# Performance work log

Hardware: AMD Instinct MI355X
Metric: run time of the kernel (lower is better)

The kernel has to match this reference:

```python
import jax, jax.numpy as jnp
import numpy as np

N_NODES = 100000


def setup_inputs() -> dict:
    key = jax.random.key(0)
    k1, k2, k3, k4, k5 = jax.random.split(key, 5)
    x = jax.random.normal(k1, (N_NODES, 256), dtype=jnp.float32)
    edge_index = jax.random.randint(k2, (2, 3200000), 0, N_NODES, dtype=jnp.int64)
    edge_weight = jax.random.uniform(k3, (3200000,), dtype=jnp.float32)
    W = jax.random.normal(k4, (256, 128), dtype=jnp.float32) / np.sqrt(256.0)
    b = jax.random.normal(k5, (128,), dtype=jnp.float32) * 0.01
    return {"x": x, "edge_index": edge_index, "edge_weight": edge_weight, "W": W, "b": b}


def reference(x, edge_index, edge_weight, W, b):
    # Dense linear projection: h = x @ W + b  -> [N, out_feats]
    h = x @ W + b
    # SpMM aggregation: out[dst] += w_e * h[src]
    src = edge_index[1]  # column indices (neighbors)
    dst = edge_index[0]  # row indices (output nodes)
    msgs = h[src] * edge_weight[:, None]  # [E, out_feats]
    out = jax.ops.segment_sum(msgs, dst, num_segments=x.shape[0])
    return out
```

## Files before the change

### kernel.cpp

```cpp
#include <hip/hip_runtime.h>

#define K_IN   256
#define N_OUT  128
#define BM     32
#define SCAN_CHUNK 1024
#define NBLK   512
#define BSHIFT 7
#define BNODES 128
#define CAP    8192
#define NKEY   2048

typedef short bf16x8 __attribute__((ext_vector_type(8)));
typedef float f32x4  __attribute__((ext_vector_type(4)));

static __device__ __forceinline__ unsigned short f2bf(float f) {
    unsigned u = __float_as_uint(f);
    unsigned r = (u + 0x7FFF + ((u >> 16) & 1)) >> 16;
    return (unsigned short)r;
}
static __device__ __forceinline__ float bf2f(unsigned short b) {
    return __uint_as_float(((unsigned)b) << 16);
}

__global__ __launch_bounds__(256) void prep_w(const float* __restrict__ W, char* __restrict__ wbt)
{
    const int t = blockIdx.x * 256 + threadIdx.x;
    if (t >= N_OUT * 32) return;
    const int n = t >> 5;
    const int c = t & 31;
    unsigned v[4];
#pragma unroll
    for (int p = 0; p < 4; ++p) {
        const unsigned lo = f2bf(W[(size_t)(c * 8 + 2 * p)     * N_OUT + n]);
        const unsigned hi = f2bf(W[(size_t)(c * 8 + 2 * p + 1) * N_OUT + n]);
        v[p] = lo | (hi << 16);
    }
    const int byte = n * 512 + ((c * 16) ^ ((n & 7) << 4));
    *reinterpret_cast<uint4*>(wbt + byte) = make_uint4(v[0], v[1], v[2], v[3]);
}

__global__ __launch_bounds__(256) void gcn_gemm(
    const float* __restrict__ x, const uint4* __restrict__ wbt,
    const float* __restrict__ bias, unsigned short* __restrict__ hb,
    const int* __restrict__ ei, int* __restrict__ histG,
    int M, int E, int B, int chunk)
{
    __shared__ uint4 smem4[81920 / 16];
    char* smem = (char*)smem4;
    const int tid  = threadIdx.x;
    const int row0 = blockIdx.x * BM;

    {
        uint4* wl = (uint4*)smem;
#pragma unroll
        for (int it = 0; it < 16; ++it) wl[it * 256 + tid] = wbt[it * 256 + tid];
    }
    {
        const int r    = tid >> 3;
        const int ks   = tid & 7;
        const int grow = row0 + r;
        char* xbase    = smem + 65536 + r * 512;
        const int swz  = (r & 7) << 4;
        if (grow < M) {
            const float4* src = reinterpret_cast<const float4*>(x + (size_t)grow * K_IN + ks * 32);
#pragma unroll
            for (int q = 0; q < 8; ++q) {
                const float4 f = src[q];
                uint2 v;
                v.x = (unsigned)f2bf(f.x) | ((unsigned)f2bf(f.y) << 16);
                v.y = (unsigned)f2bf(f.z) | ((unsigned)f2bf(f.w) << 16);
                const int kb = ks * 64 + q * 8;
                *reinterpret_cast<uint2*>(xbase + (((kb & ~15) ^ swz) | (kb & 15))) = v;
            }
        } else {
            const uint2 z = make_uint2(0u, 0u);
#pragma unroll
            for (int q = 0; q < 8; ++q) {
                const int kb = ks * 64 + q * 8;
                *reinterpret_cast<uint2*>(xbase + (((kb & ~15) ^ swz) | (kb & 15))) = z;
            }
        }
    }
    __syncthreads();

    const int lane = tid & 63;
    const int wv   = tid >> 6;
    const int wr   = wv >> 1;
    const int wc   = wv & 1;
    const int l15  = lane & 15;
    const int lk   = lane >> 4;

    const int  arow = wr * 16 + l15;
    const char* xrow = smem + 65536 + arow * 512;
    const int  aswz = (arow & 7) << 4;
    const int  bswz = (l15 & 7) << 4;
    const char* brow0 = smem + (size_t)(wc * 64 + l15) * 512;

    f32x4 acc[4] = {};

#pragma unroll
    for (int ks = 0; ks < 8; ++ks) {
        const int kb = ks * 64 + lk * 16;
        const bf16x8 a = *reinterpret_cast<const bf16x8*>(xrow + (kb ^ aswz));
        const int bk = kb ^ bswz;
#pragma unroll
        for (int j = 0; j < 4; ++j) {
            const bf16x8 b = *reinterpret_cast<const bf16x8*>(brow0 + j * (16 * 512) + bk);
            acc[j] = __builtin_amdgcn_mfma_f32_16x16x32_bf16(a, b, acc[j], 0, 0, 0);
        }
    }

#pragma unroll
    for (int j = 0; j < 4; ++j) {
        const int gcol = wc * 64 + j * 16 + l15;
        const float bv = bias[gcol];
#pragma unroll
        for (int r = 0; r < 4; ++r) {
            const int grow = row0 + wr * 16 + lk * 4 + r;
            if (grow < M)
                hb[(size_t)grow * N_OUT + gcol] = f2bf(acc[j][r] + bv);
        }
    }

    if (blockIdx.x < NBLK) {
        __syncthreads();
        int* bins = (int*)smem;
        for (int i = tid; i < B; i += 256) bins[i] = 0;
        __syncthreads();
        const int beg = blockIdx.x * chunk;
        const int end = min(beg + chunk, E);
        for (int i = beg + tid; i < end; i += 256)
            atomicAdd(&bins[ei[i] >> BSHIFT], 1);
        __syncthreads();
        for (int i = tid; i < B; i += 256) histG[i * NBLK + blockIdx.x] = bins[i];
    }
}

__global__ __launch_bounds__(256) void scan_block_sums(
    const int* __restrict__ cnt, int n, int* __restrict__ bsum)
{
    __shared__ int sd[256];
    const int base = blockIdx.x * SCAN_CHUNK + threadIdx.x * 4;
    int s = 0;
#pragma unroll
    for (int j = 0; j < 4; ++j) { const int idx = base + j; if (idx < n) s += cnt[idx]; }
    sd[threadIdx.x] = s; __syncthreads();
    for (int off = 128; off > 0; off >>= 1) {
        if (threadIdx.x < off) sd[threadIdx.x] += sd[threadIdx.x + off];
        __syncthreads();
    }
    if (threadIdx.x == 0) bsum[blockIdx.x] = sd[0];
}

__global__ __launch_bounds__(1024) void scan_sums(
    int* __restrict__ bsum, int nb, int* __restrict__ P, int n)
{
    __shared__ int sd[1024];
    const int t = threadIdx.x;
    const int v = (t < nb) ? bsum[t] : 0;
    sd[t] = v; __syncthreads();
    for (int off = 1; off < 1024; off <<= 1) {
        const int add = (t >= off) ? sd[t - off] : 0;
        __syncthreads();
        sd[t] += add;
        __syncthreads();
    }
    if (t < nb) bsum[t] = sd[t] - v;
    if (t == nb - 1) P[n] = sd[t];
}

__global__ __launch_bounds__(256) void scan_write_offsets(
    const int* __restrict__ cnt, int n, const int* __restrict__ bsum, int* __restrict__ P)
{
    __shared__ int sd[256];
    const int t = threadIdx.x;
    const int base = blockIdx.x * SCAN_CHUNK + t * 4;
    int v[4]; int s = 0;
#pragma unroll
    for (int j = 0; j < 4; ++j) { const int idx = base + j; v[j] = (idx < n) ? cnt[idx] : 0; s += v[j]; }
    sd[t] = s; __syncthreads();
    const int own = s;
    for (int off = 1; off < 256; off <<= 1) {
        const int add = (t >= off) ? sd[t - off] : 0;
        __syncthreads();
        sd[t] += add;
        __syncthreads();
    }
    int run = bsum[blockIdx.x] + (sd[t] - own);
#pragma unroll
    for (int j = 0; j < 4; ++j) {
        const int idx = base + j;
        if (idx < n) { P[idx] = run; run += v[j]; }
    }
}

__global__ __launch_bounds__(256) void scatter_records(
    const int* __restrict__ ei, const float* __restrict__ ew, int E, int M, int B,
    const int* __restrict__ P, uint2* __restrict__ rec, int chunk)
{
    __shared__ int cur[1024];
    for (int i = threadIdx.x; i < B; i += 256) cur[i] = P[i * NBLK + blockIdx.x];
    __syncthreads();
    const int beg = blockIdx.x * chunk;
    const int end = min(beg + chunk, E);
    for (int i = beg + threadIdx.x; i < end; i += 256) {
        const int d = ei[i];
        const int s = ei[(size_t)E + i];
        const int pos = atomicAdd(&cur[d >> BSHIFT], 1);
        rec[pos] = make_uint2((unsigned)s | ((unsigned)(d & (BNODES - 1)) << 24),
                              __float_as_uint(ew[i]));
    }
}

__global__ __launch_bounds__(256) void sort_bucket(
    const int* __restrict__ P, uint2* __restrict__ rec,
    int* __restrict__ offsN, int* __restrict__ bflag, int M, int B)
{
    __shared__ uint2 srt[CAP];
    __shared__ int hist[NKEY];
    __shared__ int sd[256];

    const int b   = blockIdx.x;
    const int tid = threadIdx.x;
    const int beg = P[b * NBLK];
    const int end = P[(b + 1) * NBLK];
    const int cnt = end - beg;
    const int node0 = b << BSHIFT;

    for (int i = tid; i < NKEY; i += 256) hist[i] = 0;
    if (tid == 0) bflag[b] = (cnt <= CAP) ? 0 : 1;
    if (tid == 0 && b == B - 1) offsN[M] = end;
    __syncthreads();

    if (cnt > CAP) {
        if (tid < BNODES) {
            const int node = node0 + tid;
            if (node < M) offsN[node] = beg;
        }
        return;
    }

    for (int i = beg + tid; i < end; i += 256) {
        const uint2 r = rec[i];
        srt[i - beg] = r;
        const int key = ((r.x >> 24) << 4) | ((r.x & 0xFFFFFF) >> 13);
        atomicAdd(&hist[key], 1);
    }
    __syncthreads();

    const int base = tid * 8;
    int v[8]; int s = 0;
#pragma unroll
    for (int j = 0; j < 8; ++j) { v[j] = hist[base + j]; s += v[j]; }
    sd[tid] = s; __syncthreads();
    for (int off = 1; off < 256; off <<= 1) {
        const int add = (tid >= off) ? sd[tid - off] : 0;
        __syncthreads();
        sd[tid] += add;
        __syncthreads();
    }
    int run = sd[tid] - s;
#pragma unroll
    for (int j = 0; j < 8; ++j) { hist[base + j] = run; run += v[j]; }
    __syncthreads();

    if (tid < BNODES) {
        const int node = node0 + tid;
        if (node < M) offsN[node] = beg + hist[tid << 4];
    }
    __syncthreads();

    for (int i = tid; i < cnt; i += 256) {
        const uint2 r = srt[i];
        const int key = ((r.x >> 24) << 4) | ((r.x & 0xFFFFFF) >> 13);
        const int pos = atomicAdd(&hist[key], 1);
        rec[beg + pos] = r;
    }
}

__global__ __launch_bounds__(256) void gather_kernel(
    const int* __restrict__ offsN, const int* __restrict__ P,
    const int* __restrict__ bflag, const uint2* __restrict__ rec,
    const unsigned short* __restrict__ hb, float* __restrict__ out, int M)
{
    const int n = blockIdx.x * 4 + (threadIdx.x >> 6);
    if (n >= M) return;
    const int lane = threadIdx.x & 63;
    const int b = n >> BSHIFT;
    const unsigned* __restrict__ hb32 = reinterpret_cast<const unsigned*>(hb);

    float ax = 0.f, ay = 0.f;

    if (bflag[b] == 0) {
        const int beg = offsN[n], end = offsN[n + 1];
        int i = beg;
        for (; i + 8 <= end; i += 8) {
            unsigned u[8]; float w[8];
#pragma unroll
            for (int q = 0; q < 8; ++q) {
                const uint2 r = rec[i + q];
                w[q] = __uint_as_float(r.y);
                u[q] = hb32[(size_t)((r.x & 0xFFFFFF) << 6) + lane];
            }
#pragma unroll
            for (int q = 0; q < 8; ++q) {
                ax += w[q] * bf2f((unsigned short)u[q]);
                ay += w[q] * bf2f((unsigned short)(u[q] >> 16));
            }
        }
        for (; i < end; ++i) {
            const uint2 r = rec[i];
            const float w = __uint_as_float(r.y);
            const unsigned u = hb32[(size_t)((r.x & 0xFFFFFF) << 6) + lane];
            ax += w * bf2f((unsigned short)u);
            ay += w * bf2f((unsigned short)(u >> 16));
        }
    } else {
        const int beg = P[b * NBLK], end = P[(b + 1) * NBLK];
        const unsigned want = (unsigned)(n & (BNODES - 1));
        for (int i = beg; i < end; ++i) {
            const uint2 r = rec[i];
            if ((r.x >> 24) != want) continue;
            const float w = __uint_as_float(r.y);
            const unsigned u = hb32[(size_t)((r.x & 0xFFFFFF) << 6) + lane];
            ax += w * bf2f((unsigned short)u);
            ay += w * bf2f((unsigned short)(u >> 16));
        }
    }

    reinterpret_cast<float2*>(out + (size_t)n * N_OUT)[lane] = make_float2(ax, ay);
}

extern "C" void kernel_launch(void* const* d_in, const int* in_sizes, int n_in,
                              void* d_out, int out_size, void* d_ws, size_t ws_size,
                              hipStream_t stream)
{
    const float* x    = (const float*)d_in[0];
    const int*   ei   = (const int*)d_in[1];
    const float* ew   = (const float*)d_in[2];
    const float* W    = (const float*)d_in[3];
    const float* bias = (const float*)d_in[4];
    float* out = (float*)d_out;

    const int M = in_sizes[0] / K_IN;
    const int E = in_sizes[1] / 2;
    const int B = (M + BNODES - 1) >> BSHIFT;
    const int n = B * NBLK;
    const int nb = (n + SCAN_CHUNK - 1) / SCAN_CHUNK;
    const int chunk = (E + NBLK - 1) / NBLK;

    auto align256 = [](size_t v) { return (v + 255) & ~(size_t)255; };
    const size_t o_hb    = 0;
    const size_t o_hist  = align256(o_hb + (size_t)M * N_OUT * sizeof(unsigned short));
    const size_t o_P     = align256(o_hist + (size_t)n * sizeof(int));
    const size_t o_bsum  = align256(o_P + (size_t)(n + 1) * sizeof(int));
    const size_t o_offsN = align256(o_bsum + (size_t)1024 * sizeof(int));
    const size_t o_bflag = align256(o_offsN + (size_t)(M + 1) * sizeof(int));
    const size_t o_wbt   = align256(o_bflag + (size_t)B * sizeof(int));
    const size_t o_rec   = align256(o_wbt + (size_t)65536);

    unsigned short* hb    = (unsigned short*)((char*)d_ws + o_hb);
    int*            histG = (int*)((char*)d_ws + o_hist);
    int*            P     = (int*)((char*)d_ws + o_P);
    int*            bsum  = (int*)((char*)d_ws + o_bsum);
    int*            offsN = (int*)((char*)d_ws + o_offsN);
    int*            bflag = (int*)((char*)d_ws + o_bflag);
    char*           wbt   = (char*)d_ws + o_wbt;
    uint2*          rec   = (uint2*)((char*)d_ws + o_rec);

    prep_w<<<16, 256, 0, stream>>>(W, wbt);
    gcn_gemm<<<(M + BM - 1) / BM, 256, 0, stream>>>(
        x, (const uint4*)wbt, bias, hb, ei, histG, M, E, B, chunk);
    scan_block_sums<<<nb, 256, 0, stream>>>(histG, n, bsum);
    scan_sums<<<1, 1024, 0, stream>>>(bsum, nb, P, n);
    scan_write_offsets<<<nb, 256, 0, stream>>>(histG, n, bsum, P);
    scatter_records<<<NBLK, 256, 0, stream>>>(ei, ew, E, M, B, P, rec, chunk);
    sort_bucket<<<B, 256, 0, stream>>>(P, rec, offsN, bflag, M, B);
    gather_kernel<<<(M + 3) / 4, 256, 0, stream>>>(offsN, P, bflag, rec, hb, out, M);
}
```

Baseline: 266.9 us.

## Gather per bucket with source-window ordering for cache locality

The per-node gather is replaced by one block per 128-node bucket. Each wave accumulates 32 destination nodes in registers. Work is walked by source-node windows, using per-(node,window) offsets that the sort kernel now writes to global memory. The aim is to improve cache reuse of the projected feature rows by having all waves touch the same source window together. The cost is far fewer blocks and waves, short serial per-key loops with no load batching, and higher register pressure.

```diff
diff --git a/kernel.cpp b/kernel.cpp
--- a/kernel.cpp
+++ b/kernel.cpp
@@ -9,6 +9,7 @@
 #define BNODES 128
 #define CAP    8192
 #define NKEY   2048
+#define WSHIFT 13
 
 typedef short bf16x8 __attribute__((ext_vector_type(8)));
 typedef float f32x4  __attribute__((ext_vector_type(4)));
@@ -214,7 +215,7 @@
 
 __global__ __launch_bounds__(256) void sort_bucket(
     const int* __restrict__ P, uint2* __restrict__ rec,
-    int* __restrict__ offsN, int* __restrict__ bflag, int M, int B)
+    int* __restrict__ offK, int* __restrict__ bflag, int M, int B)
 {
     __shared__ uint2 srt[CAP];
     __shared__ int hist[NKEY];
@@ -225,25 +226,17 @@
     const int beg = P[b * NBLK];
     const int end = P[(b + 1) * NBLK];
     const int cnt = end - beg;
-    const int node0 = b << BSHIFT;
 
     for (int i = tid; i < NKEY; i += 256) hist[i] = 0;
     if (tid == 0) bflag[b] = (cnt <= CAP) ? 0 : 1;
-    if (tid == 0 && b == B - 1) offsN[M] = end;
-    __syncthreads();
-
-    if (cnt > CAP) {
-        if (tid < BNODES) {
-            const int node = node0 + tid;
-            if (node < M) offsN[node] = beg;
-        }
-        return;
-    }
+    __syncthreads();
+
+    if (cnt > CAP) return;
 
     for (int i = beg + tid; i < end; i += 256) {
         const uint2 r = rec[i];
         srt[i - beg] = r;
-        const int key = ((r.x >> 24) << 4) | ((r.x & 0xFFFFFF) >> 13);
+        const int key = ((r.x >> 24) << 4) | ((r.x & 0xFFFFFF) >> WSHIFT);
         atomicAdd(&hist[key], 1);
     }
     __syncthreads();
@@ -264,71 +257,81 @@
     for (int j = 0; j < 8; ++j) { hist[base + j] = run; run += v[j]; }
     __syncthreads();
 
-    if (tid < BNODES) {
-        const int node = node0 + tid;
-        if (node < M) offsN[node] = beg + hist[tid << 4];
-    }
+    for (int i = tid; i < NKEY; i += 256)
+        offK[(size_t)b * NKEY + i] = beg + hist[i];
     __syncthreads();
 
     for (int i = tid; i < cnt; i += 256) {
         const uint2 r = srt[i];
-        const int key = ((r.x >> 24) << 4) | ((r.x & 0xFFFFFF) >> 13);
+        const int key = ((r.x >> 24) << 4) | ((r.x & 0xFFFFFF) >> WSHIFT);
         const int pos = atomicAdd(&hist[key], 1);
         rec[beg + pos] = r;
     }
 }
 
-__global__ __launch_bounds__(256) void gather_kernel(
-    const int* __restrict__ offsN, const int* __restrict__ P,
+__global__ __launch_bounds__(256) void gather_win(
+    const int* __restrict__ offK, const int* __restrict__ P,
     const int* __restrict__ bflag, const uint2* __restrict__ rec,
-    const unsigned short* __restrict__ hb, float* __restrict__ out, int M)
-{
-    const int n = blockIdx.x * 4 + (threadIdx.x >> 6);
-    if (n >= M) return;
-    const int lane = threadIdx.x & 63;
-    const int b = n >> BSHIFT;
+    const unsigned short* __restrict__ hb, float* __restrict__ out,
+    int M, int nwin)
+{
+    __shared__ int koff[NKEY];
+    const int b    = blockIdx.x;
+    const int tid  = threadIdx.x;
+    const int lane = tid & 63;
+    const int wv   = tid >> 6;
+    const int node0 = (b << BSHIFT) + wv * 32;
     const unsigned* __restrict__ hb32 = reinterpret_cast<const unsigned*>(hb);
 
-    float ax = 0.f, ay = 0.f;
+    for (int i = tid; i < NKEY; i += 256) koff[i] = offK[(size_t)b * NKEY + i];
+    __syncthreads();
+
+    float ax[32], ay[32];
+#pragma unroll
+    for (int i = 0; i < 32; ++i) { ax[i] = 0.f; ay[i] = 0.f; }
 
     if (bflag[b] == 0) {
-        const int beg = offsN[n], end = offsN[n + 1];
-        int i = beg;
-        for (; i + 8 <= end; i += 8) {
-            unsigned u[8]; float w[8];
-#pragma unroll
-            for (int q = 0; q < 8; ++q) {
-                const uint2 r = rec[i + q];
-                w[q] = __uint_as_float(r.y);
-                u[q] = hb32[(size_t)((r.x & 0xFFFFFF) << 6) + lane];
+        for (int win = 0; win < nwin; ++win) {
+#pragma unroll
+            for (int nn = 0; nn < 32; ++nn) {
+                const int key = ((wv * 32 + nn) << 4) | win;
+                const int s = koff[key];
+                const int e = koff[key + 1];
+                for (int i = s; i < e; ++i) {
+                    const uint2 r = rec[i];
+                    const float w = __uint_as_float(r.y);
+                    const unsigned u = hb32[(size_t)((r.x & 0xFFFFFF) << 6) + lane];
+                    ax[nn] += w * bf2f((unsigned short)u);
+                    ay[nn] += w * bf2f((unsigned short)(u >> 16));
+                }
             }
-#pragma unroll
-            for (int q = 0; q < 8; ++q) {
-                ax += w[q] * bf2f((unsigned short)u[q]);
-                ay += w[q] * bf2f((unsigned short)(u[q] >> 16));
-            }
-        }
-        for (; i < end; ++i) {
+            __syncthreads();
+        }
+    } else {
+        const int beg = P[b * NBLK], end = P[(b + 1) * NBLK];
+        for (int i = beg; i < end; ++i) {
             const uint2 r = rec[i];
+            const int dl = (int)(r.x >> 24);
+            if ((dl >> 5) != wv) continue;
             const float w = __uint_as_float(r.y);
             const unsigned u = hb32[(size_t)((r.x & 0xFFFFFF) << 6) + lane];
-            ax += w * bf2f((unsigned short)u);
-            ay += w * bf2f((unsigned short)(u >> 16));
-        }
-    } else {
-        const int beg = P[b * NBLK], end = P[(b + 1) * NBLK];
-        const unsigned want = (unsigned)(n & (BNODES - 1));
-        for (int i = beg; i < end; ++i) {
-            const uint2 r = rec[i];
-            if ((r.x >> 24) != want) continue;
-            const float w = __uint_as_float(r.y);
-            const unsigned u = hb32[(size_t)((r.x & 0xFFFFFF) << 6) + lane];
-            ax += w * bf2f((unsigned short)u);
-            ay += w * bf2f((unsigned short)(u >> 16));
-        }
-    }
-
-    reinterpret_cast<float2*>(out + (size_t)n * N_OUT)[lane] = make_float2(ax, ay);
+#pragma unroll
+            for (int nn = 0; nn < 32; ++nn) {
+                if (nn == (dl & 31)) {
+                    ax[nn] += w * bf2f((unsigned short)u);
+                    ay[nn] += w * bf2f((unsigned short)(u >> 16));
+                }
+            }
+        }
+    }
+
+#pragma unroll
+    for (int nn = 0; nn < 32; ++nn) {
+        const int node = node0 + nn;
+        if (node < M)
+            reinterpret_cast<float2*>(out + (size_t)node * N_OUT)[lane] =
+                make_float2(ax[nn], ay[nn]);
+    }
 }
 
 extern "C" void kernel_launch(void* const* d_in, const int* in_sizes, int n_in,
@@ -348,14 +351,15 @@
     const int n = B * NBLK;
     const int nb = (n + SCAN_CHUNK - 1) / SCAN_CHUNK;
     const int chunk = (E + NBLK - 1) / NBLK;
+    const int nwin = (M + (1 << WSHIFT) - 1) >> WSHIFT;
 
     auto align256 = [](size_t v) { return (v + 255) & ~(size_t)255; };
     const size_t o_hb    = 0;
     const size_t o_hist  = align256(o_hb + (size_t)M * N_OUT * sizeof(unsigned short));
     const size_t o_P     = align256(o_hist + (size_t)n * sizeof(int));
     const size_t o_bsum  = align256(o_P + (size_t)(n + 1) * sizeof(int));
-    const size_t o_offsN = align256(o_bsum + (size_t)1024 * sizeof(int));
-    const size_t o_bflag = align256(o_offsN + (size_t)(M + 1) * sizeof(int));
+    const size_t o_offK  = align256(o_bsum + (size_t)1024 * sizeof(int));
+    const size_t o_bflag = align256(o_offK + (size_t)B * NKEY * sizeof(int));
     const size_t o_wbt   = align256(o_bflag + (size_t)B * sizeof(int));
     const size_t o_rec   = align256(o_wbt + (size_t)65536);
 
@@ -363,7 +367,7 @@
     int*            histG = (int*)((char*)d_ws + o_hist);
     int*            P     = (int*)((char*)d_ws + o_P);
     int*            bsum  = (int*)((char*)d_ws + o_bsum);
-    int*            offsN = (int*)((char*)d_ws + o_offsN);
+    int*            offK  = (int*)((char*)d_ws + o_offK);
     int*            bflag = (int*)((char*)d_ws + o_bflag);
     char*           wbt   = (char*)d_ws + o_wbt;
     uint2*          rec   = (uint2*)((char*)d_ws + o_rec);
@@ -375,6 +379,6 @@
     scan_sums<<<1, 1024, 0, stream>>>(bsum, nb, P, n);
     scan_write_offsets<<<nb, 256, 0, stream>>>(histG, n, bsum, P);
     scatter_records<<<NBLK, 256, 0, stream>>>(ei, ew, E, M, B, P, rec, chunk);
-    sort_bucket<<<B, 256, 0, stream>>>(P, rec, offsN, bflag, M, B);
-    gather_kernel<<<(M + 3) / 4, 256, 0, stream>>>(offsN, P, bflag, rec, hb, out, M);
-}
+    sort_bucket<<<B, 256, 0, stream>>>(P, rec, offK, bflag, M, B);
+    gather_win<<<B, 256, 0, stream>>>(offK, P, bflag, rec, hb, out, M, nwin);
+}
```

Result: slower. 711.0 us (+166.4%).
